# Kernel tuning notes

Hardware: AMD Instinct MI355X
Metric: run time of the kernel (lower is better)

Reference implementation:

```python
import jax, jax.numpy as jnp
import numpy as np

N, S, E, H = 4, 2048, 1024, 16
D = E // H


def setup_inputs() -> dict:
    key = jax.random.key(0)
    ks = jax.random.split(key, 12)
    s = 1.0 / np.sqrt(E)  # torch Linear default init scale-ish
    inp = {
        "value": jax.random.normal(ks[0], (N, S, E), jnp.float32),
        "key": jax.random.normal(ks[1], (N, S, E), jnp.float32),
        "query": jax.random.normal(ks[2], (N, S, E), jnp.float32),
        "mask": jax.random.randint(ks[3], (N, 1, S, S), 0, 2, dtype=jnp.int32),
        "Wv": jax.random.normal(ks[4], (E, E), jnp.float32) * s,
        "bv": jax.random.normal(ks[5], (E,), jnp.float32) * s,
        "Wk": jax.random.normal(ks[6], (E, E), jnp.float32) * s,
        "bk": jax.random.normal(ks[7], (E,), jnp.float32) * s,
        "Wq": jax.random.normal(ks[8], (E, E), jnp.float32) * s,
        "bq": jax.random.normal(ks[9], (E,), jnp.float32) * s,
        "Wo": jax.random.normal(ks[10], (E, E), jnp.float32) * s,
        "bo": jax.random.normal(ks[11], (E,), jnp.float32) * s,
    }
    return inp


def reference(value, key, query, mask, Wv, bv, Wk, bk, Wq, bq, Wo, bo):
    n, q_len = query.shape[0], query.shape[1]
    v = (value @ Wv.T + bv).reshape(n, -1, H, D)
    k = (key @ Wk.T + bk).reshape(n, -1, H, D)
    q = (query @ Wq.T + bq).reshape(n, -1, H, D)
    qk = jnp.einsum('nqhd,nkhd->nhqk', q, k)  # [N,H,Q,K]
    # faithful quirk: masked positions set to 1e-20 (not -inf), BEFORE scaling
    qk = jnp.where(mask == 0, jnp.asarray(1e-20, qk.dtype), qk)
    attn = jax.nn.softmax(qk / jnp.asarray(np.sqrt(E), qk.dtype), axis=3)
    out = jnp.einsum('nhqk,nkhd->nqhd', attn, v).reshape(n, q_len, H * D)
    return out @ Wo.T + bo
```

## Files before the change

kernel.cpp:

```cpp
#include <hip/hip_runtime.h>
#include <stdint.h>

typedef unsigned short u16;
typedef __bf16 bf16x8 __attribute__((ext_vector_type(8)));
typedef float f32x4 __attribute__((ext_vector_type(4)));

#define SN 4
#define SS 2048
#define SE 1024
#define SH 16
#define SD 64

__device__ __forceinline__ u16 f2bf(float f) {
    unsigned u = __builtin_bit_cast(unsigned, f);
    unsigned r = u + 0x7FFF + ((u >> 16) & 1);
    return (u16)(r >> 16);
}

__device__ __forceinline__ u16 f2bf_fast(float f) {
    unsigned u = __builtin_bit_cast(unsigned, f);
    return (u16)((u + 0x8000) >> 16);
}

__device__ __forceinline__ void gload_lds16(const void* g, void* l) {
    __builtin_amdgcn_global_load_lds((__attribute__((address_space(1))) void*)(g),
                                     (__attribute__((address_space(3))) void*)(l),
                                     16, 0, 0);
}

__global__ __launch_bounds__(256) void cvt_bf16(const float* __restrict__ in,
                                                u16* __restrict__ out, int n8) {
    int i = blockIdx.x * blockDim.x + threadIdx.x;
    if (i >= n8) return;
    float4 a = ((const float4*)in)[i * 2];
    float4 b = ((const float4*)in)[i * 2 + 1];
    uint4 o;
    o.x = (unsigned)f2bf(a.x) | ((unsigned)f2bf(a.y) << 16);
    o.y = (unsigned)f2bf(a.z) | ((unsigned)f2bf(a.w) << 16);
    o.z = (unsigned)f2bf(b.x) | ((unsigned)f2bf(b.y) << 16);
    o.w = (unsigned)f2bf(b.z) | ((unsigned)f2bf(b.w) << 16);
    ((uint4*)out)[i] = o;
}

__global__ __launch_bounds__(256) void mask_pack(const int* __restrict__ m,
                                                 unsigned long long* __restrict__ out,
                                                 int nwords) {
    int lane = threadIdx.x & 63;
    int wid = (blockIdx.x * blockDim.x + threadIdx.x) >> 6;
    int nw = (gridDim.x * blockDim.x) >> 6;
    for (int w = wid; w < nwords; w += nw) {
        int v = m[(size_t)w * 64 + lane];
        unsigned long long b = __ballot(v != 0);
        if (lane == 0) out[w] = b;
    }
}

template <int OUTF32>
__global__ __launch_bounds__(256, 4) void gemm_bt(const u16* __restrict__ A,
                                                  const u16* __restrict__ W,
                                                  const float* __restrict__ bias,
                                                  void* __restrict__ C,
                                                  int M, int K, int NC) {
    __shared__ __align__(16) u16 sA[2][128 * 32];
    __shared__ __align__(16) u16 sB[2][128 * 32];
    const int tid = threadIdx.x;
    const int wv = tid >> 6, lane = tid & 63;
    const int wr = wv >> 1, wc = wv & 1;
    const int l15 = lane & 15, lhi = lane >> 4;
    const int rowBase = blockIdx.x * 128, colBase = blockIdx.y * 128;

    f32x4 acc[4][4] = {};
    const int NT = K / 32;

    auto stage = [&](int buf, int kt) {
        int k0 = kt * 32;
#pragma unroll
        for (int i = 0; i < 2; i++) {
            int t = i * 256 + tid;
            int r = t >> 2, c = t & 3;
            gload_lds16(A + (size_t)(rowBase + r) * K + k0 + c * 8,
                        &sA[buf][(i * 256 + wv * 64) * 8]);
            gload_lds16(W + (size_t)(colBase + r) * K + k0 + c * 8,
                        &sB[buf][(i * 256 + wv * 64) * 8]);
        }
    };

    stage(0, 0);
    __syncthreads();
    int buf = 0;
    for (int kt = 0; kt < NT; ++kt) {
        if (kt + 1 < NT) stage(buf ^ 1, kt + 1);
        bf16x8 af[4], bfr[4];
#pragma unroll
        for (int mt = 0; mt < 4; ++mt) {
            int ra = wr * 64 + mt * 16 + l15;
            af[mt] = *(const bf16x8*)&sA[buf][ra * 32 + lhi * 8];
        }
#pragma unroll
        for (int nt = 0; nt < 4; ++nt) {
            int rb = wc * 64 + nt * 16 + l15;
            bfr[nt] = *(const bf16x8*)&sB[buf][rb * 32 + lhi * 8];
        }
#pragma unroll
        for (int mt = 0; mt < 4; ++mt)
#pragma unroll
            for (int nt = 0; nt < 4; ++nt)
                acc[mt][nt] = __builtin_amdgcn_mfma_f32_16x16x32_bf16(
                    af[mt], bfr[nt], acc[mt][nt], 0, 0, 0);
        __syncthreads();
        buf ^= 1;
    }

#pragma unroll
    for (int mt = 0; mt < 4; ++mt) {
#pragma unroll
        for (int nt = 0; nt < 4; ++nt) {
            int col = colBase + wc * 64 + nt * 16 + l15;
            float bcol = bias[col];
#pragma unroll
            for (int r = 0; r < 4; ++r) {
                int row = rowBase + wr * 64 + mt * 16 + lhi * 4 + r;
                float v = acc[mt][nt][r] + bcol;
                if (OUTF32)
                    ((float*)C)[(size_t)row * NC + col] = v;
                else
                    ((u16*)C)[(size_t)row * NC + col] = f2bf(v);
            }
        }
    }
}

__global__ __launch_bounds__(256, 4) void gemm_qkv(
    const u16* __restrict__ xq, const u16* __restrict__ xk, const u16* __restrict__ xv,
    const u16* __restrict__ wq, const u16* __restrict__ wk, const u16* __restrict__ wv,
    const float* __restrict__ bq, const float* __restrict__ bk, const float* __restrict__ bv,
    u16* __restrict__ qb, u16* __restrict__ kb, u16* __restrict__ vb) {
    const int K = SE, NC = SE;
    int flat = blockIdx.x;
    int z = flat >> 9;
    int s = flat & 511;
    int x = s & 63, y = s >> 6;
    const u16* A = (z == 0) ? xq : (z == 1) ? xk : xv;
    const u16* W = (z == 0) ? wq : (z == 1) ? wk : wv;
    const float* bias = (z == 0) ? bq : (z == 1) ? bk : bv;
    u16* C = (z == 0) ? qb : (z == 1) ? kb : vb;

    __shared__ __align__(16) u16 sA[2][128 * 32];
    __shared__ __align__(16) u16 sB[2][128 * 32];
    const int tid = threadIdx.x;
    const int wv_ = tid >> 6, lane = tid & 63;
    const int wr = wv_ >> 1, wc = wv_ & 1;
    const int l15 = lane & 15, lhi = lane >> 4;
    const int rowBase = x * 128, colBase = y * 128;

    f32x4 acc[4][4] = {};
    const int NT = K / 32;

    auto stage = [&](int buf, int kt) {
        int k0 = kt * 32;
#pragma unroll
        for (int i = 0; i < 2; i++) {
            int t = i * 256 + tid;
            int r = t >> 2, c = t & 3;
            gload_lds16(A + (size_t)(rowBase + r) * K + k0 + c * 8,
                        &sA[buf][(i * 256 + wv_ * 64) * 8]);
            gload_lds16(W + (size_t)(colBase + r) * K + k0 + c * 8,
                        &sB[buf][(i * 256 + wv_ * 64) * 8]);
        }
    };

    stage(0, 0);
    __syncthreads();
    int buf = 0;
    for (int kt = 0; kt < NT; ++kt) {
        if (kt + 1 < NT) stage(buf ^ 1, kt + 1);
        bf16x8 af[4], bfr[4];
#pragma unroll
        for (int mt = 0; mt < 4; ++mt) {
            int ra = wr * 64 + mt * 16 + l15;
            af[mt] = *(const bf16x8*)&sA[buf][ra * 32 + lhi * 8];
        }
#pragma unroll
        for (int nt = 0; nt < 4; ++nt) {
            int rb = wc * 64 + nt * 16 + l15;
            bfr[nt] = *(const bf16x8*)&sB[buf][rb * 32 + lhi * 8];
        }
#pragma unroll
        for (int mt = 0; mt < 4; ++mt)
#pragma unroll
            for (int nt = 0; nt < 4; ++nt)
                acc[mt][nt] = __builtin_amdgcn_mfma_f32_16x16x32_bf16(
                    af[mt], bfr[nt], acc[mt][nt], 0, 0, 0);
        __syncthreads();
        buf ^= 1;
    }

#pragma unroll
    for (int mt = 0; mt < 4; ++mt) {
#pragma unroll
        for (int nt = 0; nt < 4; ++nt) {
            int col = colBase + wc * 64 + nt * 16 + l15;
            float bcol = bias[col];
#pragma unroll
            for (int r = 0; r < 4; ++r) {
                int row = rowBase + wr * 64 + mt * 16 + lhi * 4 + r;
                float v = acc[mt][nt][r] + bcol;
                C[(size_t)row * NC + col] = f2bf(v);
            }
        }
    }
}

__global__ __launch_bounds__(256) void vtrans(const u16* __restrict__ V,
                                              u16* __restrict__ VT) {
    __shared__ __align__(16) u16 tile[64][80];
    int b = blockIdx.x;
    int st = b & 31, h = (b >> 5) & 15, n = b >> 9;
    int tid = threadIdx.x;
#pragma unroll
    for (int i = 0; i < 2; i++) {
        int t = i * 256 + tid;
        int r = t >> 3, c = t & 7;
        *(uint4*)&tile[r][c * 8] =
            *(const uint4*)(V + ((size_t)(n * SS + st * 64 + r) * SE + h * 64 + c * 8));
    }
    __syncthreads();
#pragma unroll
    for (int i = 0; i < 2; i++) {
        int t = i * 256 + tid;
        int d = t >> 3, c = t & 7;
        u16 tmp[8];
#pragma unroll
        for (int j = 0; j < 8; j++) tmp[j] = tile[c * 8 + j][d];
        *(uint4*)(VT + ((size_t)((n * SH + h) * SD + d) * SS + st * 64 + c * 8)) =
            *(const uint4*)tmp;
    }
}

__global__ __launch_bounds__(256, 4) void attn(const u16* __restrict__ Qm,
                                               const u16* __restrict__ Km,
                                               const u16* __restrict__ VTm,
                                               const unsigned long long* __restrict__ M64,
                                               u16* __restrict__ Om) {
    __shared__ __align__(16) u16 kl[2][64 * 64];
    __shared__ __align__(16) u16 vl[2][64 * 64];
    __shared__ __align__(16) u16 pl[128 * 64];
    int tid = threadIdx.x, wv = tid >> 6, lane = tid & 63;
    int b = blockIdx.x;
    int qt = b & 15, h = (b >> 4) & 15, n = b >> 8;
    int q0 = qt * 128;
    const int l15 = lane & 15, lhi = lane >> 4;

    bf16x8 qf[2][2];
#pragma unroll
    for (int mt = 0; mt < 2; ++mt)
#pragma unroll
        for (int kk = 0; kk < 2; ++kk)
            qf[mt][kk] = *(const bf16x8*)(Qm +
                ((size_t)(n * SS + q0 + wv * 32 + mt * 16 + l15) * SE + h * 64 +
                 kk * 32 + lhi * 8));

    float lsum[2][4] = {};
    f32x4 oacc[2][4] = {};

    auto stage = [&](int buf, int t) {
#pragma unroll
        for (int i = 0; i < 2; i++) {
            int tt = i * 256 + tid;
            int r = tt >> 3, c = tt & 7;
            int cs = c ^ (r & 7);
            gload_lds16(Km + ((size_t)(n * SS + t * 64 + r) * SE + h * 64 + cs * 8),
                        &kl[buf][(i * 256 + wv * 64) * 8]);
            gload_lds16(VTm + ((size_t)((n * SH + h) * SD + r) * SS + t * 64 + cs * 8),
                        &vl[buf][(i * 256 + wv * 64) * 8]);
        }
    };

    stage(0, 0);
    __syncthreads();
    int buf = 0;
    const float C2 = 0.04508422f;
    const int sw = l15 & 7;
    const size_t mbase = ((size_t)(n * SS + q0 + wv * 32 + lhi * 4)) * 32;
    for (int t = 0; t < 32; ++t) {
        if (t + 1 < 32) stage(buf ^ 1, t + 1);
        unsigned long long mw0[4];
#pragma unroll
        for (int r = 0; r < 4; ++r) mw0[r] = M64[mbase + (size_t)r * 32 + t];
        f32x4 sac[2][4] = {};
        __builtin_amdgcn_s_setprio(1);
#pragma unroll
        for (int kk = 0; kk < 2; ++kk) {
            bf16x8 kf[4];
#pragma unroll
            for (int nt = 0; nt < 4; ++nt) {
                int row = nt * 16 + l15;
                int cg = (kk * 4 + lhi) ^ sw;
                kf[nt] = *(const bf16x8*)&kl[buf][row * 64 + cg * 8];
            }
#pragma unroll
            for (int mt = 0; mt < 2; ++mt)
#pragma unroll
                for (int nt = 0; nt < 4; ++nt)
                    sac[mt][nt] = __builtin_amdgcn_mfma_f32_16x16x32_bf16(
                        qf[mt][kk], kf[nt], sac[mt][nt], 0, 0, 0);
        }
        __builtin_amdgcn_s_setprio(0);
        unsigned long long mw1[4];
#pragma unroll
        for (int r = 0; r < 4; ++r) mw1[r] = M64[mbase + (size_t)(16 + r) * 32 + t];
#pragma unroll
        for (int mt = 0; mt < 2; ++mt) {
#pragma unroll
            for (int r = 0; r < 4; ++r) {
                unsigned long long m = (mt == 0) ? mw0[r] : mw1[r];
                float p[4];
#pragma unroll
                for (int nt = 0; nt < 4; ++nt) {
                    int cb = nt * 16 + l15;
                    float e = __builtin_amdgcn_exp2f(sac[mt][nt][r] * C2);
                    p[nt] = ((m >> cb) & 1ull) ? e : 1.0f;
                }
                lsum[mt][r] += (p[0] + p[1]) + (p[2] + p[3]);
                int prow = wv * 32 + mt * 16 + lhi * 4 + r;
                int psw = prow & 7;
#pragma unroll
                for (int nt = 0; nt < 4; ++nt) {
                    int cg = ((nt * 2) + (l15 >> 3)) ^ psw;
                    pl[prow * 64 + cg * 8 + (l15 & 7)] = f2bf_fast(p[nt]);
                }
            }
        }
        __builtin_amdgcn_s_setprio(1);
#pragma unroll
        for (int kk = 0; kk < 2; ++kk) {
            bf16x8 pa[2], vbf[4];
#pragma unroll
            for (int mt = 0; mt < 2; ++mt) {
                int row = wv * 32 + mt * 16 + l15;
                int cg = (kk * 4 + lhi) ^ sw;
                pa[mt] = *(const bf16x8*)&pl[row * 64 + cg * 8];
            }
#pragma unroll
            for (int nt = 0; nt < 4; ++nt) {
                int row = nt * 16 + l15;
                int cg = (kk * 4 + lhi) ^ sw;
                vbf[nt] = *(const bf16x8*)&vl[buf][row * 64 + cg * 8];
            }
#pragma unroll
            for (int mt = 0; mt < 2; ++mt)
#pragma unroll
                for (int nt = 0; nt < 4; ++nt)
                    oacc[mt][nt] = __builtin_amdgcn_mfma_f32_16x16x32_bf16(
                        pa[mt], vbf[nt], oacc[mt][nt], 0, 0, 0);
        }
        __builtin_amdgcn_s_setprio(0);
        __syncthreads();
        buf ^= 1;
    }
#pragma unroll
    for (int mt = 0; mt < 2; ++mt) {
#pragma unroll
        for (int r = 0; r < 4; ++r) {
            float ls = lsum[mt][r];
#pragma unroll
            for (int d = 1; d < 16; d <<= 1) ls += __shfl_xor(ls, d);
            float inv = 1.0f / ls;
            size_t row = (size_t)(n * SS + q0 + wv * 32 + mt * 16 + lhi * 4 + r);
#pragma unroll
            for (int nt = 0; nt < 4; ++nt) {
                float v = oacc[mt][nt][r] * inv;
                Om[row * SE + h * 64 + nt * 16 + l15] = f2bf(v);
            }
        }
    }
}

extern "C" void kernel_launch(void* const* d_in, const int* in_sizes, int n_in,
                              void* d_out, int out_size, void* d_ws, size_t ws_size,
                              hipStream_t stream) {
    const float* value = (const float*)d_in[0];
    const float* key = (const float*)d_in[1];
    const float* query = (const float*)d_in[2];
    const int* mask = (const int*)d_in[3];
    const float* Wv = (const float*)d_in[4];
    const float* bv = (const float*)d_in[5];
    const float* Wk = (const float*)d_in[6];
    const float* bk = (const float*)d_in[7];
    const float* Wq = (const float*)d_in[8];
    const float* bq = (const float*)d_in[9];
    const float* Wo = (const float*)d_in[10];
    const float* bo = (const float*)d_in[11];
    float* out = (float*)d_out;

    char* ws = (char*)d_ws;
    const size_t XB = (size_t)8192 * 1024 * 2;
    const size_t WB = (size_t)1024 * 1024 * 2;
    u16* xv = (u16*)(ws);
    u16* xk = (u16*)(ws + XB);
    u16* xq = (u16*)(ws + 2 * XB);
    u16* wv_ = (u16*)(ws + 3 * XB);
    u16* wk_ = (u16*)(ws + 3 * XB + WB);
    u16* wq_ = (u16*)(ws + 3 * XB + 2 * WB);
    u16* wo_ = (u16*)(ws + 3 * XB + 3 * WB);
    u16* qb = (u16*)(ws + 3 * XB + 4 * WB);
    u16* kb = (u16*)(ws + 4 * XB + 4 * WB);
    u16* vbuf = (u16*)(ws + 5 * XB + 4 * WB);
    unsigned long long* m64 = (unsigned long long*)(ws + 6 * XB + 4 * WB);
    u16* vt = xv;
    u16* ob = xk;

    cvt_bf16<<<4096, 256, 0, stream>>>(value, xv, 1048576);
    cvt_bf16<<<4096, 256, 0, stream>>>(key, xk, 1048576);
    cvt_bf16<<<4096, 256, 0, stream>>>(query, xq, 1048576);
    cvt_bf16<<<512, 256, 0, stream>>>(Wv, wv_, 131072);
    cvt_bf16<<<512, 256, 0, stream>>>(Wk, wk_, 131072);
    cvt_bf16<<<512, 256, 0, stream>>>(Wq, wq_, 131072);
    cvt_bf16<<<512, 256, 0, stream>>>(Wo, wo_, 131072);
    mask_pack<<<2048, 256, 0, stream>>>(mask, m64, SN * SS * (SS / 64));

    gemm_qkv<<<1536, 256, 0, stream>>>(xq, xk, xv, wq_, wk_, wv_, bq, bk, bv,
                                       qb, kb, vbuf);
    vtrans<<<2048, 256, 0, stream>>>(vbuf, vt);
    attn<<<1024, 256, 0, stream>>>(qb, kb, vt, m64, ob);
    dim3 g(64, 8, 1);
    gemm_bt<1><<<g, 256, 0, stream>>>(ob, wo_, bo, out, 8192, 1024, 1024);
}
```

Before: 469.3 us.

## Keep softmax probabilities in registers using transposed 32x32 MFMA scores

Result: faster. 448.2 us (-4.5%).

```diff
diff --git a/kernel.cpp b/kernel.cpp
--- a/kernel.cpp
+++ b/kernel.cpp
@@ -4,6 +4,7 @@
 typedef unsigned short u16;
 typedef __bf16 bf16x8 __attribute__((ext_vector_type(8)));
 typedef float f32x4 __attribute__((ext_vector_type(4)));
+typedef float f32x16 __attribute__((ext_vector_type(16)));
 
 #define SN 4
 #define SS 2048
@@ -17,9 +18,10 @@
     return (u16)(r >> 16);
 }
 
-__device__ __forceinline__ u16 f2bf_fast(float f) {
-    unsigned u = __builtin_bit_cast(unsigned, f);
-    return (u16)((u + 0x8000) >> 16);
+__device__ __forceinline__ unsigned pk2bf(float a, float b) {
+    unsigned ua = __builtin_bit_cast(unsigned, a) + 0x8000u;
+    unsigned ub = __builtin_bit_cast(unsigned, b) + 0x8000u;
+    return (ub & 0xffff0000u) | (ua >> 16);
 }
 
 __device__ __forceinline__ void gload_lds16(const void* g, void* l) {
@@ -244,24 +246,21 @@
                                                u16* __restrict__ Om) {
     __shared__ __align__(16) u16 kl[2][64 * 64];
     __shared__ __align__(16) u16 vl[2][64 * 64];
-    __shared__ __align__(16) u16 pl[128 * 64];
     int tid = threadIdx.x, wv = tid >> 6, lane = tid & 63;
     int b = blockIdx.x;
     int qt = b & 15, h = (b >> 4) & 15, n = b >> 8;
     int q0 = qt * 128;
-    const int l15 = lane & 15, lhi = lane >> 4;
-
-    bf16x8 qf[2][2];
-#pragma unroll
-    for (int mt = 0; mt < 2; ++mt)
-#pragma unroll
-        for (int kk = 0; kk < 2; ++kk)
-            qf[mt][kk] = *(const bf16x8*)(Qm +
-                ((size_t)(n * SS + q0 + wv * 32 + mt * 16 + l15) * SE + h * 64 +
-                 kk * 32 + lhi * 8));
-
-    float lsum[2][4] = {};
-    f32x4 oacc[2][4] = {};
+    const int l31 = lane & 31, hi = lane >> 5;
+    const int qrow = q0 + wv * 32 + l31;
+
+    bf16x8 qf[4];
+#pragma unroll
+    for (int dstep = 0; dstep < 4; ++dstep)
+        qf[dstep] = *(const bf16x8*)(Qm + (size_t)(n * SS + qrow) * SE + h * 64 +
+                                     dstep * 16 + hi * 8);
+
+    float lsum = 0.f;
+    f32x16 oacc[2] = {};
 
     auto stage = [&](int buf, int t) {
 #pragma unroll
@@ -280,99 +279,76 @@
     __syncthreads();
     int buf = 0;
     const float C2 = 0.04508422f;
-    const int sw = l15 & 7;
-    const size_t mbase = ((size_t)(n * SS + q0 + wv * 32 + lhi * 4)) * 32;
+    const int rsw = l31 & 7;
+    const size_t mrow = (size_t)(n * SS + qrow) * 32;
     for (int t = 0; t < 32; ++t) {
         if (t + 1 < 32) stage(buf ^ 1, t + 1);
-        unsigned long long mw0[4];
-#pragma unroll
-        for (int r = 0; r < 4; ++r) mw0[r] = M64[mbase + (size_t)r * 32 + t];
-        f32x4 sac[2][4] = {};
+        unsigned long long mws = M64[mrow + t] >> (hi * 4);
+        f32x16 st[2] = {};
         __builtin_amdgcn_s_setprio(1);
 #pragma unroll
-        for (int kk = 0; kk < 2; ++kk) {
-            bf16x8 kf[4];
-#pragma unroll
-            for (int nt = 0; nt < 4; ++nt) {
-                int row = nt * 16 + l15;
-                int cg = (kk * 4 + lhi) ^ sw;
-                kf[nt] = *(const bf16x8*)&kl[buf][row * 64 + cg * 8];
+        for (int dstep = 0; dstep < 4; ++dstep) {
+            int cg = (dstep * 2 + hi) ^ rsw;
+            bf16x8 a0 = *(const bf16x8*)&kl[buf][(l31)*64 + cg * 8];
+            bf16x8 a1 = *(const bf16x8*)&kl[buf][(32 + l31) * 64 + cg * 8];
+            st[0] = __builtin_amdgcn_mfma_f32_32x32x16_bf16(a0, qf[dstep], st[0], 0, 0, 0);
+            st[1] = __builtin_amdgcn_mfma_f32_32x32x16_bf16(a1, qf[dstep], st[1], 0, 0, 0);
+        }
+        __builtin_amdgcn_s_setprio(0);
+        bf16x8 pfrag[4];
+#pragma unroll
+        for (int kt = 0; kt < 2; ++kt) {
+            float p[16];
+#pragma unroll
+            for (int r = 0; r < 16; ++r) {
+                int bit = kt * 32 + (r & 3) + 8 * (r >> 2);
+                float e = __builtin_amdgcn_exp2f(st[kt][r] * C2);
+                p[r] = ((mws >> bit) & 1ull) ? e : 1.0f;
             }
-#pragma unroll
-            for (int mt = 0; mt < 2; ++mt)
-#pragma unroll
-                for (int nt = 0; nt < 4; ++nt)
-                    sac[mt][nt] = __builtin_amdgcn_mfma_f32_16x16x32_bf16(
-                        qf[mt][kk], kf[nt], sac[mt][nt], 0, 0, 0);
-        }
-        __builtin_amdgcn_s_setprio(0);
-        unsigned long long mw1[4];
-#pragma unroll
-        for (int r = 0; r < 4; ++r) mw1[r] = M64[mbase + (size_t)(16 + r) * 32 + t];
-#pragma unroll
-        for (int mt = 0; mt < 2; ++mt) {
-#pragma unroll
-            for (int r = 0; r < 4; ++r) {
-                unsigned long long m = (mt == 0) ? mw0[r] : mw1[r];
-                float p[4];
-#pragma unroll
-                for (int nt = 0; nt < 4; ++nt) {
-                    int cb = nt * 16 + l15;
-                    float e = __builtin_amdgcn_exp2f(sac[mt][nt][r] * C2);
-                    p[nt] = ((m >> cb) & 1ull) ? e : 1.0f;
-                }
-                lsum[mt][r] += (p[0] + p[1]) + (p[2] + p[3]);
-                int prow = wv * 32 + mt * 16 + lhi * 4 + r;
-                int psw = prow & 7;
-#pragma unroll
-                for (int nt = 0; nt < 4; ++nt) {
-                    int cg = ((nt * 2) + (l15 >> 3)) ^ psw;
-                    pl[prow * 64 + cg * 8 + (l15 & 7)] = f2bf_fast(p[nt]);
-                }
+            lsum += ((p[0] + p[1]) + (p[2] + p[3])) + ((p[4] + p[5]) + (p[6] + p[7])) +
+                    (((p[8] + p[9]) + (p[10] + p[11])) + ((p[12] + p[13]) + (p[14] + p[15])));
+#pragma unroll
+            for (int klo = 0; klo < 2; ++klo) {
+                unsigned w0 = pk2bf(p[8 * klo + 0], p[8 * klo + 1]);
+                unsigned w1 = pk2bf(p[8 * klo + 2], p[8 * klo + 3]);
+                unsigned w2 = pk2bf(p[8 * klo + 4], p[8 * klo + 5]);
+                unsigned w3 = pk2bf(p[8 * klo + 6], p[8 * klo + 7]);
+                unsigned sx0 = (unsigned)__shfl_xor((int)w0, 32);
+                unsigned sx1 = (unsigned)__shfl_xor((int)w1, 32);
+                unsigned sx2 = (unsigned)__shfl_xor((int)w2, 32);
+                unsigned sx3 = (unsigned)__shfl_xor((int)w3, 32);
+                uint4 f;
+                f.x = hi ? sx2 : w0;
+                f.y = hi ? sx3 : w1;
+                f.z = hi ? w2 : sx0;
+                f.w = hi ? w3 : sx1;
+                pfrag[kt * 2 + klo] = __builtin_bit_cast(bf16x8, f);
             }
         }
         __builtin_amdgcn_s_setprio(1);
 #pragma unroll
-        for (int kk = 0; kk < 2; ++kk) {
-            bf16x8 pa[2], vbf[4];
-#pragma unroll
-            for (int mt = 0; mt < 2; ++mt) {
-                int row = wv * 32 + mt * 16 + l15;
-                int cg = (kk * 4 + lhi) ^ sw;
-                pa[mt] = *(const bf16x8*)&pl[row * 64 + cg * 8];
+        for (int nt = 0; nt < 2; ++nt) {
+#pragma unroll
+            for (int ks = 0; ks < 4; ++ks) {
+                int cg = (ks * 2 + hi) ^ rsw;
+                bf16x8 vb = *(const bf16x8*)&vl[buf][(nt * 32 + l31) * 64 + cg * 8];
+                oacc[nt] = __builtin_amdgcn_mfma_f32_32x32x16_bf16(pfrag[ks], vb,
+                                                                   oacc[nt], 0, 0, 0);
             }
-#pragma unroll
-            for (int nt = 0; nt < 4; ++nt) {
-                int row = nt * 16 + l15;
-                int cg = (kk * 4 + lhi) ^ sw;
-                vbf[nt] = *(const bf16x8*)&vl[buf][row * 64 + cg * 8];
-            }
-#pragma unroll
-            for (int mt = 0; mt < 2; ++mt)
-#pragma unroll
-                for (int nt = 0; nt < 4; ++nt)
-                    oacc[mt][nt] = __builtin_amdgcn_mfma_f32_16x16x32_bf16(
-                        pa[mt], vbf[nt], oacc[mt][nt], 0, 0, 0);
         }
         __builtin_amdgcn_s_setprio(0);
         __syncthreads();
         buf ^= 1;
     }
-#pragma unroll
-    for (int mt = 0; mt < 2; ++mt) {
-#pragma unroll
-        for (int r = 0; r < 4; ++r) {
-            float ls = lsum[mt][r];
-#pragma unroll
-            for (int d = 1; d < 16; d <<= 1) ls += __shfl_xor(ls, d);
-            float inv = 1.0f / ls;
-            size_t row = (size_t)(n * SS + q0 + wv * 32 + mt * 16 + lhi * 4 + r);
-#pragma unroll
-            for (int nt = 0; nt < 4; ++nt) {
-                float v = oacc[mt][nt][r] * inv;
-                Om[row * SE + h * 64 + nt * 16 + l15] = f2bf(v);
-            }
-        }
+    float lst = lsum + __shfl_xor(lsum, 32);
+    float inv = 1.0f / lst;
+#pragma unroll
+    for (int r = 0; r < 16; ++r) {
+        int crow = (r & 3) + 8 * (r >> 2) + 4 * hi;
+        float invq = __shfl(inv, crow);
+        size_t row = (size_t)(n * SS + q0 + wv * 32 + crow);
+        Om[row * SE + h * 64 + l31] = f2bf(oacc[0][r] * invq);
+        Om[row * SE + h * 64 + 32 + l31] = f2bf(oacc[1][r] * invq);
     }
 }
 
```
